# Kernel tuning notes

Hardware: AMD Instinct MI355X
Metric: run time of the kernel (lower is better)

The kernel has to match this reference:

```python
import jax, jax.numpy as jnp
import numpy as np
import math

B, W, C, N = 4, 2048, 1024, 16
K = C // N  # 64


def setup_inputs() -> dict:
    key = jax.random.key(0)
    k1, k2, k3, k4, k5 = jax.random.split(key, 5)
    return {
        "in_sequence_bwc": jax.random.normal(k1, (B, W, C), dtype=jnp.float32),
        "W_proj": jax.random.normal(k2, (C, C), dtype=jnp.float32) * 0.02,   # torch Linear weight [out,in]
        "pre_metric_nkk": jax.random.normal(k3, (N, K, K), dtype=jnp.float32) * 0.1,
        "transforms_nkk": jax.random.normal(k4, (N, K, K), dtype=jnp.float32) * 0.1,
        "W_mixer": jax.random.normal(k5, (C, C), dtype=jnp.float32) * 0.02,
    }


def reference(in_sequence_bwc, W_proj, pre_metric_nkk, transforms_nkk, W_mixer):
    b, w, c = in_sequence_bwc.shape
    # metric tensor per head: M = P P^T (positive semidefinite-ish bilinear form)
    metric_nkk = jnp.einsum("nij,nkj->nik", pre_metric_nkk, pre_metric_nkk)
    # shared projection (torch Linear: x @ W^T)
    proj_bwc = in_sequence_bwc @ W_proj.T
    proj_bnwk = proj_bwc.reshape(b, w, N, K).transpose(0, 2, 1, 3)  # [b,n,w,k]
    # bilinear scores Q M Q^T / sqrt(k)
    qm_bnwk = jnp.einsum("bnwk,nkj->bnwj", proj_bnwk, metric_nkk)
    scores_bnww = jnp.einsum("bnwk,bnvk->bnwv", qm_bnwk, proj_bnwk) / math.sqrt(K)
    # multiplicative causal mask (no softmax)
    mask_ww = jnp.tril(jnp.ones((w, w), dtype=scores_bnww.dtype))
    scores_bnww = scores_bnww * mask_ww
    # nudged = scores @ proj @ T per head
    nudged_bnwk = jnp.einsum("bnwv,bnvk->bnwk", scores_bnww, proj_bnwk)
    nudged_bnwk = jnp.einsum("bnwk,nkj->bnwj", nudged_bnwk, transforms_nkk)
    nudged_bwc = nudged_bnwk.transpose(0, 2, 1, 3).reshape(b, w, c)
    return nudged_bwc @ W_mixer.T
```

## Files before the change

kernel.cpp:

```cpp
#include <hip/hip_runtime.h>

#define B_ 4
#define W_ 2048
#define C_ 1024
#define NH 16
#define KH 64

typedef __attribute__((ext_vector_type(8))) short short8;
typedef __attribute__((ext_vector_type(4))) short s16x4;
typedef __attribute__((ext_vector_type(4))) float f32x4;

__device__ __forceinline__ short f2bf(float f) {
    unsigned u = __builtin_bit_cast(unsigned, f);
    u = (u + 0x7FFFu + ((u >> 16) & 1u)) >> 16;
    return (short)u;
}
__device__ __forceinline__ float bf2f(short h) {
    return __builtin_bit_cast(float, ((unsigned)(unsigned short)h) << 16);
}

#define MFMA(a, b, cc) __builtin_amdgcn_mfma_f32_16x16x32_bf16(a, b, cc, 0, 0, 0)

__global__ __launch_bounds__(256) void k_prep(const float* __restrict__ x, const float* __restrict__ Wp,
                                              const float* __restrict__ Pm, const float* __restrict__ Tr,
                                              const float* __restrict__ Wm,
                                              short* __restrict__ x16, short* __restrict__ wp16,
                                              short* __restrict__ wf16, float* __restrict__ metric) {
    int bid = blockIdx.x, t = threadIdx.x;
    __shared__ float sA[KH * 65];
    __shared__ float sB[KH * KH];
    if (bid < 1152) {
        const float4* src;
        short4* dst;
        int base;
        if (bid < 1024) { src = (const float4*)x;  dst = (short4*)x16;  base = bid * 2048 + t; }
        else            { src = (const float4*)Wp; dst = (short4*)wp16; base = (bid - 1024) * 2048 + t; }
        float4 v[8];
        #pragma unroll
        for (int e = 0; e < 8; ++e) v[e] = src[base + e * 256];
        #pragma unroll
        for (int e = 0; e < 8; ++e) {
            short4 o;
            o.x = f2bf(v[e].x); o.y = f2bf(v[e].y); o.z = f2bf(v[e].z); o.w = f2bf(v[e].w);
            dst[base + e * 256] = o;
        }
    } else if (bid < 1408) {
        int idx = bid - 1152;
        int oseg = idx & 15, n = idx >> 4;
        for (int i = t; i < KH * KH; i += 256) {
            sA[(i & 63) * 65 + (i >> 6)] = Tr[n * KH * KH + i];
            int r = i >> 6, c = i & 63;
            sB[i] = Wm[(oseg * KH + r) * C_ + n * KH + c];
        }
        __syncthreads();
        for (int e = t; e < KH * KH; e += 256) {
            int r = e >> 6, k = e & 63;
            float s = 0.f;
            #pragma unroll 8
            for (int j = 0; j < KH; ++j) s += sA[j * 65 + k] * sB[r * KH + j];
            wf16[(oseg * KH + r) * C_ + n * KH + k] = f2bf(s);
        }
    } else {
        int n = bid - 1408;
        const float* Pn = Pm + n * KH * KH;
        for (int i = t; i < KH * KH; i += 256) {
            float v = Pn[i];
            sB[i] = v;
            sA[(i & 63) * 65 + (i >> 6)] = v;
        }
        __syncthreads();
        float* Mn = metric + n * KH * KH;
        for (int e = t; e < KH * KH; e += 256) {
            int i = e >> 6, k = e & 63;
            float s = 0.f;
            #pragma unroll 8
            for (int j = 0; j < KH; ++j) s += sB[i * KH + j] * sA[j * 65 + k];
            Mn[e] = s;
        }
    }
}

template <int OC, int STRIDE, bool OUT_FP32>
__global__ __launch_bounds__(256) void k_gemm(const short* __restrict__ A, const short* __restrict__ Bw,
                                              void* __restrict__ Out) {
    __shared__ short As[128 * 64];
    __shared__ short Bs[64 * 64];
    constexpr int NBX = OC / 64;
    int id = blockIdx.x + blockIdx.y * NBX;
    int fl = (id & 7) * (NBX * 64 / 8) + (id >> 3);
    int bm = fl / NBX, bn = fl % NBX;
    int t = threadIdx.x;
    int wave = t >> 6, lane = t & 63;
    int q = lane >> 4, c = lane & 15;
    int wy = wave >> 1, wx = wave & 1;
    f32x4 acc[4][2] = {};
    int xsw = (c & 7);
    for (int k0 = 0; k0 < C_; k0 += 64) {
        __syncthreads();
        #pragma unroll
        for (int e = 0; e < 4; ++e) {
            int row = (e * 256 + t) >> 3;
            int ks = ((t & 7) ^ (row & 7)) * 8;
            __builtin_amdgcn_global_load_lds(
                (const __attribute__((address_space(1))) void*)&A[(size_t)(bm * 128 + row) * C_ + k0 + ks],
                (__attribute__((address_space(3))) void*)&As[e * 2048 + wave * 512], 16, 0, 0);
        }
        #pragma unroll
        for (int e = 0; e < 2; ++e) {
            int row = (e * 256 + t) >> 3;
            int ks = ((t & 7) ^ (row & 7)) * 8;
            __builtin_amdgcn_global_load_lds(
                (const __attribute__((address_space(1))) void*)&Bw[(size_t)(bn * 64 + row) * C_ + k0 + ks],
                (__attribute__((address_space(3))) void*)&Bs[e * 2048 + wave * 512], 16, 0, 0);
        }
        __syncthreads();
        #pragma unroll
        for (int kk = 0; kk < 64; kk += 32) {
            int o = kk >> 3;
            int xo = ((o + q) ^ xsw) * 8;
            short8 af[4], bfr[2];
            #pragma unroll
            for (int i = 0; i < 4; ++i)
                af[i] = *(const short8*)&As[(wy * 64 + i * 16 + c) * 64 + xo];
            #pragma unroll
            for (int j = 0; j < 2; ++j)
                bfr[j] = *(const short8*)&Bs[(wx * 32 + j * 16 + c) * 64 + xo];
            #pragma unroll
            for (int i = 0; i < 4; ++i)
                #pragma unroll
                for (int j = 0; j < 2; ++j)
                    acc[i][j] = MFMA(af[i], bfr[j], acc[i][j]);
        }
    }
    #pragma unroll
    for (int i = 0; i < 4; ++i)
        #pragma unroll
        for (int j = 0; j < 2; ++j)
            #pragma unroll
            for (int r = 0; r < 4; ++r) {
                int row = bm * 128 + wy * 64 + i * 16 + q * 4 + r;
                int col = bn * 64 + wx * 32 + j * 16 + c;
                if (OUT_FP32) ((float*)Out)[(size_t)row * STRIDE + col] = acc[i][j][r];
                else ((short*)Out)[(size_t)row * STRIDE + col] = f2bf(acc[i][j][r]);
            }
}

__global__ __launch_bounds__(256) void k_outer(short* __restrict__ pjqm,
                                               const float* __restrict__ metric,
                                               short* __restrict__ Chi, short* __restrict__ Clo) {
    int cc = blockIdx.x, n = blockIdx.y, b = blockIdx.z;
    int bn = b * NH + n;
    int t = threadIdx.x, wave = t >> 6, lane = t & 63;
    int q = lane >> 4, c = lane & 15;
    int w0g = b * W_ + cc * 64;
    __shared__ short Pt_s[64 * 72];
    __shared__ short Mb[64 * 72];

    const float* Mn = metric + n * 4096;
    #pragma unroll
    for (int e = 0; e < 4; ++e) {
        int i4 = e * 256 + t;
        float4 v = ((const float4*)Mn)[i4];
        s16x4 o;
        o[0] = f2bf(v.x * 0.125f); o[1] = f2bf(v.y * 0.125f);
        o[2] = f2bf(v.z * 0.125f); o[3] = f2bf(v.w * 0.125f);
        int row = i4 >> 4, col = (i4 & 15) * 4;
        *(s16x4*)&Mb[row * 72 + col] = o;
    }
    if (cc < 31) {
        #pragma unroll
        for (int e = 0; e < 2; ++e) {
            int chv = e * 256 + t, row = chv >> 3, sub = chv & 7;
            short8 p8 = *(const short8*)&pjqm[(size_t)(w0g + row) * 2048 + n * KH + sub * 8];
            #pragma unroll
            for (int j = 0; j < 8; ++j) Pt_s[(sub * 8 + j) * 72 + row] = p8[j];
        }
    }
    __syncthreads();

    {
        const short* arow = &pjqm[(size_t)(w0g + wave * 16 + c) * 2048 + n * KH];
        short8 a0 = *(const short8*)(arow + q * 8);
        short8 a1 = *(const short8*)(arow + 32 + q * 8);
        #pragma unroll
        for (int ct = 0; ct < 4; ++ct) {
            short8 b0 = *(const short8*)&Mb[(ct * 16 + c) * 72 + q * 8];
            short8 b1 = *(const short8*)&Mb[(ct * 16 + c) * 72 + 32 + q * 8];
            f32x4 acc = {};
            acc = MFMA(a0, b0, acc);
            acc = MFMA(a1, b1, acc);
            #pragma unroll
            for (int r = 0; r < 4; ++r)
                pjqm[(size_t)(w0g + wave * 16 + q * 4 + r) * 2048 + 1024 + n * KH + ct * 16 + c] =
                    f2bf(acc[r]);
        }
    }

    if (cc < 31) {
        short8 a0 = *(const short8*)&Pt_s[(wave * 16 + c) * 72 + q * 8];
        short8 a1 = *(const short8*)&Pt_s[(wave * 16 + c) * 72 + 32 + q * 8];
        size_t cbase = ((size_t)bn * 32 + cc) * 4096;
        #pragma unroll
        for (int tj = 0; tj < 4; ++tj) {
            short8 b0 = *(const short8*)&Pt_s[(tj * 16 + c) * 72 + q * 8];
            short8 b1 = *(const short8*)&Pt_s[(tj * 16 + c) * 72 + 32 + q * 8];
            f32x4 acc = {};
            acc = MFMA(a0, b0, acc);
            acc = MFMA(a1, b1, acc);
            s16x4 hi, lo;
            #pragma unroll
            for (int r = 0; r < 4; ++r) {
                float a = acc[r];
                short h = f2bf(a);
                hi[r] = h;
                lo[r] = f2bf(a - bf2f(h));
            }
            size_t off = cbase + (size_t)(tj * 16 + c) * 64 + wave * 16 + q * 4;
            *(s16x4*)&Chi[off] = hi;
            *(s16x4*)&Clo[off] = lo;
        }
    }
}

__global__ __launch_bounds__(256) void k_scan(short* __restrict__ Chi, short* __restrict__ Clo) {
    int bn = blockIdx.y;
    int el = blockIdx.x * 1024 + threadIdx.x * 4;
    size_t off = (size_t)bn * 32 * 4096 + el;
    float run[4] = {0.f, 0.f, 0.f, 0.f};
    s16x4 h = *(const s16x4*)&Chi[off];
    s16x4 l = *(const s16x4*)&Clo[off];
    for (int cc = 0; cc < 31; ++cc) {
        s16x4 nh, nl;
        if (cc < 30) {
            nh = *(const s16x4*)&Chi[off + 4096];
            nl = *(const s16x4*)&Clo[off + 4096];
        }
        s16x4 oh, ol;
        #pragma unroll
        for (int r = 0; r < 4; ++r) {
            float o = bf2f(h[r]) + bf2f(l[r]);
            float cv = run[r];
            short hh = f2bf(cv);
            oh[r] = hh;
            ol[r] = f2bf(cv - bf2f(hh));
            run[r] = cv + o;
        }
        *(s16x4*)&Chi[off] = oh;
        *(s16x4*)&Clo[off] = ol;
        h = nh; l = nl;
        off += 4096;
    }
    s16x4 oh, ol;
    #pragma unroll
    for (int r = 0; r < 4; ++r) {
        short hh = f2bf(run[r]);
        oh[r] = hh;
        ol[r] = f2bf(run[r] - bf2f(hh));
    }
    *(s16x4*)&Chi[off] = oh;
    *(s16x4*)&Clo[off] = ol;
}

__global__ __launch_bounds__(256) void k_chunk(const short* __restrict__ pjqm,
                                               const short* __restrict__ Chi, const short* __restrict__ Clo,
                                               short* __restrict__ Nd) {
    int cc = blockIdx.x, n = blockIdx.y, b = blockIdx.z;
    int t = threadIdx.x, wave = t >> 6, lane = t & 63;
    int q = lane >> 4, c = lane & 15;
    __shared__ short Ps[64 * 72];
    __shared__ short Pt_s[64 * 72];
    __shared__ short Ch[64 * 72];
    __shared__ short Cl[64 * 72];
    __shared__ short St[4][16 * 72];
    int w0g = b * W_ + cc * 64;

    const short* qmrow = &pjqm[(size_t)(w0g + wave * 16 + c) * 2048 + 1024 + n * KH];
    short8 bq0 = *(const short8*)(qmrow + q * 8);
    short8 bq1 = *(const short8*)(qmrow + 32 + q * 8);

    #pragma unroll
    for (int e = 0; e < 2; ++e) {
        int chv = e * 256 + t, row = chv >> 3, sub = chv & 7;
        short8 p8 = *(const short8*)&pjqm[(size_t)(w0g + row) * 2048 + n * KH + sub * 8];
        *(short8*)&Ps[row * 72 + sub * 8] = p8;
        #pragma unroll
        for (int j = 0; j < 8; ++j) Pt_s[(sub * 8 + j) * 72 + row] = p8[j];
        size_t cbase = ((size_t)((b * NH + n) * 32 + cc)) * 4096;
        *(short8*)&Ch[row * 72 + sub * 8] = *(const short8*)&Chi[cbase + row * 64 + sub * 8];
        *(short8*)&Cl[row * 72 + sub * 8] = *(const short8*)&Clo[cbase + row * 64 + sub * 8];
    }
    __syncthreads();
    #pragma unroll
    for (int ct = 0; ct < 4; ++ct) {
        short8 a0 = *(const short8*)&Ps[(ct * 16 + c) * 72 + q * 8];
        short8 a1 = *(const short8*)&Ps[(ct * 16 + c) * 72 + 32 + q * 8];
        f32x4 s = {};
        s = MFMA(a0, bq0, s);
        s = MFMA(a1, bq1, s);
        int vb = ct * 16 + q * 4, wl = wave * 16 + c;
        s16x4 pk;
        #pragma unroll
        for (int r = 0; r < 4; ++r) {
            float v = s[r];
            if (vb + r > wl) v = 0.f;
            pk[r] = f2bf(v);
        }
        *(s16x4*)&St[wave][c * 72 + ct * 16 + q * 4] = pk;
    }
    __syncthreads();
    f32x4 oc[4] = {};
    short8 as0 = *(const short8*)&St[wave][c * 72 + q * 8];
    short8 as1 = *(const short8*)&St[wave][c * 72 + 32 + q * 8];
    #pragma unroll
    for (int tj = 0; tj < 4; ++tj) {
        short8 bp0 = *(const short8*)&Pt_s[(tj * 16 + c) * 72 + q * 8];
        short8 bp1 = *(const short8*)&Pt_s[(tj * 16 + c) * 72 + 32 + q * 8];
        oc[tj] = MFMA(as0, bp0, oc[tj]);
        oc[tj] = MFMA(as1, bp1, oc[tj]);
        short8 bh0 = *(const short8*)&Ch[(tj * 16 + c) * 72 + q * 8];
        short8 bh1 = *(const short8*)&Ch[(tj * 16 + c) * 72 + 32 + q * 8];
        oc[tj] = MFMA(bq0, bh0, oc[tj]);
        oc[tj] = MFMA(bq1, bh1, oc[tj]);
        short8 bl0 = *(const short8*)&Cl[(tj * 16 + c) * 72 + q * 8];
        short8 bl1 = *(const short8*)&Cl[(tj * 16 + c) * 72 + 32 + q * 8];
        oc[tj] = MFMA(bq0, bl0, oc[tj]);
        oc[tj] = MFMA(bq1, bl1, oc[tj]);
    }
    #pragma unroll
    for (int tj = 0; tj < 4; ++tj)
        #pragma unroll
        for (int r = 0; r < 4; ++r)
            Nd[(size_t)(w0g + wave * 16 + q * 4 + r) * C_ + n * KH + tj * 16 + c] = f2bf(oc[tj][r]);
}

extern "C" void kernel_launch(void* const* d_in, const int* in_sizes, int n_in,
                              void* d_out, int out_size, void* d_ws, size_t ws_size,
                              hipStream_t stream) {
    const float* x  = (const float*)d_in[0];
    const float* Wp = (const float*)d_in[1];
    const float* Pm = (const float*)d_in[2];
    const float* Tr = (const float*)d_in[3];
    const float* Wm = (const float*)d_in[4];
    float* out = (float*)d_out;
    char* ws = (char*)d_ws;

    const size_t MB = 1024 * 1024;
    float* metric = (float*)ws;
    short* wp16  = (short*)(ws + 256 * 1024);
    short* wf16  = (short*)(ws + 256 * 1024 + 4 * MB);
    short* x16   = (short*)(ws + 256 * 1024 + 6 * MB);
    short* pjqm  = (short*)(ws + 256 * 1024 + 22 * MB);
    short* nd16  = x16;
    short* Chi   = (short*)d_out;
    short* Clo   = Chi + 8 * MB;

    k_prep<<<dim3(1424), dim3(256), 0, stream>>>(x, Wp, Pm, Tr, Wm, x16, wp16, wf16, metric);
    k_gemm<1024, 2048, false><<<dim3(16, 64), dim3(256), 0, stream>>>(x16, wp16, (void*)pjqm);
    k_outer<<<dim3(32, NH, B_), dim3(256), 0, stream>>>(pjqm, metric, Chi, Clo);
    k_scan<<<dim3(4, 64), dim3(256), 0, stream>>>(Chi, Clo);
    k_chunk<<<dim3(32, NH, B_), dim3(256), 0, stream>>>(pjqm, Chi, Clo, nd16);
    k_gemm<1024, 1024, true><<<dim3(16, 64), dim3(256), 0, stream>>>(nd16, wf16, (void*)out);
}
```

Measured before the change: 202.1 us.

## Fuse per-chunk outer products and QM projection into projection GEMM epilogue

The separate k_outer kernel is removed, and its work moves into the epilogue of the projection GEMM. Each 128-row by 64-column tile computes Q·M for its rows and the P^T P chunk outer products for its two 64-row chunks, reading back the bf16 projection it just wrote to global memory. The scan kernel also prefetches two chunks ahead instead of one. This saves a kernel launch and a pass over pjqm, but it adds epilogue work and register pressure to the GEMM, and its correctness relies on the block's own global writes being visible after __syncthreads.

```diff
diff --git a/kernel.cpp b/kernel.cpp
--- a/kernel.cpp
+++ b/kernel.cpp
@@ -80,9 +80,10 @@
     }
 }
 
-template <int OC, int STRIDE, bool OUT_FP32>
+template <int OC, int STRIDE, bool OUT_FP32, bool DO_OUTER>
 __global__ __launch_bounds__(256) void k_gemm(const short* __restrict__ A, const short* __restrict__ Bw,
-                                              void* __restrict__ Out) {
+                                              void* __restrict__ Out, const float* __restrict__ metric,
+                                              short* __restrict__ Chi, short* __restrict__ Clo) {
     __shared__ short As[128 * 64];
     __shared__ short Bs[64 * 64];
     constexpr int NBX = OC / 64;
@@ -143,81 +144,115 @@
                 if (OUT_FP32) ((float*)Out)[(size_t)row * STRIDE + col] = acc[i][j][r];
                 else ((short*)Out)[(size_t)row * STRIDE + col] = f2bf(acc[i][j][r]);
             }
-}
-
-__global__ __launch_bounds__(256) void k_outer(short* __restrict__ pjqm,
-                                               const float* __restrict__ metric,
-                                               short* __restrict__ Chi, short* __restrict__ Clo) {
-    int cc = blockIdx.x, n = blockIdx.y, b = blockIdx.z;
-    int bn = b * NH + n;
-    int t = threadIdx.x, wave = t >> 6, lane = t & 63;
-    int q = lane >> 4, c = lane & 15;
-    int w0g = b * W_ + cc * 64;
-    __shared__ short Pt_s[64 * 72];
-    __shared__ short Mb[64 * 72];
-
-    const float* Mn = metric + n * 4096;
-    #pragma unroll
-    for (int e = 0; e < 4; ++e) {
-        int i4 = e * 256 + t;
-        float4 v = ((const float4*)Mn)[i4];
-        s16x4 o;
-        o[0] = f2bf(v.x * 0.125f); o[1] = f2bf(v.y * 0.125f);
-        o[2] = f2bf(v.z * 0.125f); o[3] = f2bf(v.w * 0.125f);
-        int row = i4 >> 4, col = (i4 & 15) * 4;
-        *(s16x4*)&Mb[row * 72 + col] = o;
-    }
-    if (cc < 31) {
+
+    if constexpr (DO_OUTER) {
+        const short* pj = (const short*)Out;
+        short* pjm = (short*)Out;
+        short* Pt = As;
+        int n = bn;
+        int Rbase = bm * 128;
+        int b = Rbase >> 11;
+        int ccA = (Rbase & (W_ - 1)) >> 6;
+        size_t bnI = (size_t)(b * NH + n);
+        const float* Mn = metric + n * 4096;
+        short8 mb0[4], mb1[4];
+        #pragma unroll
+        for (int ct = 0; ct < 4; ++ct) {
+            const float4* mrow = (const float4*)(Mn + (ct * 16 + c) * 64);
+            float4 v0 = mrow[q * 2], v1 = mrow[q * 2 + 1];
+            float4 v2 = mrow[8 + q * 2], v3 = mrow[8 + q * 2 + 1];
+            short8 m0, m1;
+            m0[0] = f2bf(v0.x * 0.125f); m0[1] = f2bf(v0.y * 0.125f);
+            m0[2] = f2bf(v0.z * 0.125f); m0[3] = f2bf(v0.w * 0.125f);
+            m0[4] = f2bf(v1.x * 0.125f); m0[5] = f2bf(v1.y * 0.125f);
+            m0[6] = f2bf(v1.z * 0.125f); m0[7] = f2bf(v1.w * 0.125f);
+            m1[0] = f2bf(v2.x * 0.125f); m1[1] = f2bf(v2.y * 0.125f);
+            m1[2] = f2bf(v2.z * 0.125f); m1[3] = f2bf(v2.w * 0.125f);
+            m1[4] = f2bf(v3.x * 0.125f); m1[5] = f2bf(v3.y * 0.125f);
+            m1[6] = f2bf(v3.z * 0.125f); m1[7] = f2bf(v3.w * 0.125f);
+            mb0[ct] = m0; mb1[ct] = m1;
+        }
+        __syncthreads();
         #pragma unroll
         for (int e = 0; e < 2; ++e) {
             int chv = e * 256 + t, row = chv >> 3, sub = chv & 7;
-            short8 p8 = *(const short8*)&pjqm[(size_t)(w0g + row) * 2048 + n * KH + sub * 8];
-            #pragma unroll
-            for (int j = 0; j < 8; ++j) Pt_s[(sub * 8 + j) * 72 + row] = p8[j];
-        }
-    }
-    __syncthreads();
-
-    {
-        const short* arow = &pjqm[(size_t)(w0g + wave * 16 + c) * 2048 + n * KH];
-        short8 a0 = *(const short8*)(arow + q * 8);
-        short8 a1 = *(const short8*)(arow + 32 + q * 8);
-        #pragma unroll
-        for (int ct = 0; ct < 4; ++ct) {
-            short8 b0 = *(const short8*)&Mb[(ct * 16 + c) * 72 + q * 8];
-            short8 b1 = *(const short8*)&Mb[(ct * 16 + c) * 72 + 32 + q * 8];
-            f32x4 acc = {};
-            acc = MFMA(a0, b0, acc);
-            acc = MFMA(a1, b1, acc);
-            #pragma unroll
-            for (int r = 0; r < 4; ++r)
-                pjqm[(size_t)(w0g + wave * 16 + q * 4 + r) * 2048 + 1024 + n * KH + ct * 16 + c] =
-                    f2bf(acc[r]);
-        }
-    }
-
-    if (cc < 31) {
-        short8 a0 = *(const short8*)&Pt_s[(wave * 16 + c) * 72 + q * 8];
-        short8 a1 = *(const short8*)&Pt_s[(wave * 16 + c) * 72 + 32 + q * 8];
-        size_t cbase = ((size_t)bn * 32 + cc) * 4096;
-        #pragma unroll
-        for (int tj = 0; tj < 4; ++tj) {
-            short8 b0 = *(const short8*)&Pt_s[(tj * 16 + c) * 72 + q * 8];
-            short8 b1 = *(const short8*)&Pt_s[(tj * 16 + c) * 72 + 32 + q * 8];
-            f32x4 acc = {};
-            acc = MFMA(a0, b0, acc);
-            acc = MFMA(a1, b1, acc);
-            s16x4 hi, lo;
-            #pragma unroll
-            for (int r = 0; r < 4; ++r) {
-                float a = acc[r];
-                short h = f2bf(a);
-                hi[r] = h;
-                lo[r] = f2bf(a - bf2f(h));
+            short8 p8 = *(const short8*)&pj[(size_t)(Rbase + row) * STRIDE + n * 64 + sub * 8];
+            #pragma unroll
+            for (int j = 0; j < 8; ++j) Pt[(sub * 8 + j) * 72 + row] = p8[j];
+        }
+        __syncthreads();
+        #pragma unroll
+        for (int s = 0; s < 2; ++s) {
+            int vrow = Rbase + wave * 32 + s * 16;
+            const short* arow = pj + (size_t)(vrow + c) * STRIDE + n * 64;
+            short8 a0 = *(const short8*)(arow + q * 8);
+            short8 a1 = *(const short8*)(arow + 32 + q * 8);
+            #pragma unroll
+            for (int ct = 0; ct < 4; ++ct) {
+                f32x4 qa = {};
+                qa = MFMA(a0, mb0[ct], qa);
+                qa = MFMA(a1, mb1[ct], qa);
+                #pragma unroll
+                for (int r = 0; r < 4; ++r)
+                    pjm[(size_t)(vrow + q * 4 + r) * STRIDE + 1024 + n * 64 + ct * 16 + c] = f2bf(qa[r]);
             }
-            size_t off = cbase + (size_t)(tj * 16 + c) * 64 + wave * 16 + q * 4;
-            *(s16x4*)&Chi[off] = hi;
-            *(s16x4*)&Clo[off] = lo;
+        }
+        {
+            short8 a0 = *(const short8*)&Pt[(wave * 16 + c) * 72 + q * 8];
+            short8 a1 = *(const short8*)&Pt[(wave * 16 + c) * 72 + 32 + q * 8];
+            size_t cbase = (bnI * 32 + ccA) * 4096;
+            #pragma unroll
+            for (int tj = 0; tj < 4; ++tj) {
+                short8 b0 = *(const short8*)&Pt[(tj * 16 + c) * 72 + q * 8];
+                short8 b1 = *(const short8*)&Pt[(tj * 16 + c) * 72 + 32 + q * 8];
+                f32x4 oa = {};
+                oa = MFMA(a0, b0, oa);
+                oa = MFMA(a1, b1, oa);
+                s16x4 hi, lo;
+                #pragma unroll
+                for (int r = 0; r < 4; ++r) {
+                    float a = oa[r];
+                    short hh = f2bf(a);
+                    hi[r] = hh;
+                    lo[r] = f2bf(a - bf2f(hh));
+                }
+                size_t off2 = cbase + (size_t)(tj * 16 + c) * 64 + wave * 16 + q * 4;
+                *(s16x4*)&Chi[off2] = hi;
+                *(s16x4*)&Clo[off2] = lo;
+            }
+        }
+        __syncthreads();
+        #pragma unroll
+        for (int e = 0; e < 2; ++e) {
+            int chv = e * 256 + t, row = chv >> 3, sub = chv & 7;
+            short8 p8 = *(const short8*)&pj[(size_t)(Rbase + 64 + row) * STRIDE + n * 64 + sub * 8];
+            #pragma unroll
+            for (int j = 0; j < 8; ++j) Pt[(sub * 8 + j) * 72 + row] = p8[j];
+        }
+        __syncthreads();
+        if (ccA + 1 < 31) {
+            short8 a0 = *(const short8*)&Pt[(wave * 16 + c) * 72 + q * 8];
+            short8 a1 = *(const short8*)&Pt[(wave * 16 + c) * 72 + 32 + q * 8];
+            size_t cbase = (bnI * 32 + ccA + 1) * 4096;
+            #pragma unroll
+            for (int tj = 0; tj < 4; ++tj) {
+                short8 b0 = *(const short8*)&Pt[(tj * 16 + c) * 72 + q * 8];
+                short8 b1 = *(const short8*)&Pt[(tj * 16 + c) * 72 + 32 + q * 8];
+                f32x4 oa = {};
+                oa = MFMA(a0, b0, oa);
+                oa = MFMA(a1, b1, oa);
+                s16x4 hi, lo;
+                #pragma unroll
+                for (int r = 0; r < 4; ++r) {
+                    float a = oa[r];
+                    short hh = f2bf(a);
+                    hi[r] = hh;
+                    lo[r] = f2bf(a - bf2f(hh));
+                }
+                size_t off2 = cbase + (size_t)(tj * 16 + c) * 64 + wave * 16 + q * 4;
+                *(s16x4*)&Chi[off2] = hi;
+                *(s16x4*)&Clo[off2] = lo;
+            }
         }
     }
 }
@@ -227,18 +262,20 @@
     int el = blockIdx.x * 1024 + threadIdx.x * 4;
     size_t off = (size_t)bn * 32 * 4096 + el;
     float run[4] = {0.f, 0.f, 0.f, 0.f};
-    s16x4 h = *(const s16x4*)&Chi[off];
-    s16x4 l = *(const s16x4*)&Clo[off];
+    s16x4 h0 = *(const s16x4*)&Chi[off];
+    s16x4 l0 = *(const s16x4*)&Clo[off];
+    s16x4 h1 = *(const s16x4*)&Chi[off + 4096];
+    s16x4 l1 = *(const s16x4*)&Clo[off + 4096];
     for (int cc = 0; cc < 31; ++cc) {
         s16x4 nh, nl;
-        if (cc < 30) {
-            nh = *(const s16x4*)&Chi[off + 4096];
-            nl = *(const s16x4*)&Clo[off + 4096];
+        if (cc < 29) {
+            nh = *(const s16x4*)&Chi[off + 8192];
+            nl = *(const s16x4*)&Clo[off + 8192];
         }
         s16x4 oh, ol;
         #pragma unroll
         for (int r = 0; r < 4; ++r) {
-            float o = bf2f(h[r]) + bf2f(l[r]);
+            float o = bf2f(h0[r]) + bf2f(l0[r]);
             float cv = run[r];
             short hh = f2bf(cv);
             oh[r] = hh;
@@ -247,7 +284,7 @@
         }
         *(s16x4*)&Chi[off] = oh;
         *(s16x4*)&Clo[off] = ol;
-        h = nh; l = nl;
+        h0 = h1; l0 = l1; h1 = nh; l1 = nl;
         off += 4096;
     }
     s16x4 oh, ol;
@@ -355,9 +392,10 @@
     short* Clo   = Chi + 8 * MB;
 
     k_prep<<<dim3(1424), dim3(256), 0, stream>>>(x, Wp, Pm, Tr, Wm, x16, wp16, wf16, metric);
-    k_gemm<1024, 2048, false><<<dim3(16, 64), dim3(256), 0, stream>>>(x16, wp16, (void*)pjqm);
-    k_outer<<<dim3(32, NH, B_), dim3(256), 0, stream>>>(pjqm, metric, Chi, Clo);
+    k_gemm<1024, 2048, false, true><<<dim3(16, 64), dim3(256), 0, stream>>>(
+        x16, wp16, (void*)pjqm, metric, Chi, Clo);
     k_scan<<<dim3(4, 64), dim3(256), 0, stream>>>(Chi, Clo);
     k_chunk<<<dim3(32, NH, B_), dim3(256), 0, stream>>>(pjqm, Chi, Clo, nd16);
-    k_gemm<1024, 1024, true><<<dim3(16, 64), dim3(256), 0, stream>>>(nd16, wf16, (void*)out);
-}
+    k_gemm<1024, 1024, true, false><<<dim3(16, 64), dim3(256), 0, stream>>>(
+        nd16, wf16, (void*)out, nullptr, nullptr, nullptr);
+}
```

Measured after the change: 210.1 us. 4.0% more time.
